# Kernel tuning notes

Hardware: AMD Instinct MI355X
Metric: run time of the kernel (lower is better)

The kernel has to match this reference:

```python
import jax, jax.numpy as jnp
import numpy as np

N = 100000   # nodes
E = 1600000  # edges (avg degree 16)
D = 128      # input_dim == output_dim (residual requires equality)
BN_EPS = 1e-5


def setup_inputs() -> dict:
    key = jax.random.key(0)
    ks = jax.random.split(key, 8)
    X = jax.random.normal(ks[0], (N, D), dtype=jnp.float32)
    E_X = jax.random.normal(ks[1], (E, D), dtype=jnp.float32)
    snorm_n = jax.random.uniform(ks[2], (N, 1), dtype=jnp.float32)
    snorm_e = jax.random.uniform(ks[3], (E, 1), dtype=jnp.float32)
    src = jax.random.randint(ks[4], (E,), 0, N, dtype=jnp.int32)
    dst = jax.random.randint(ks[5], (E,), 0, N, dtype=jnp.int32)
    # Linear A and B parameters (torch nn.Linear: y = x @ W.T + b)
    scale = 1.0 / np.sqrt(D)
    A_w = jax.random.uniform(ks[6], (D, D), dtype=jnp.float32, minval=-scale, maxval=scale)
    B_w = jax.random.uniform(ks[7], (D, D), dtype=jnp.float32, minval=-scale, maxval=scale)
    A_b = jnp.zeros((D,), jnp.float32)
    B_b = jnp.zeros((D,), jnp.float32)
    # BatchNorm1d affine params (training mode -> batch stats)
    gamma = jnp.ones((D,), jnp.float32)
    beta = jnp.zeros((D,), jnp.float32)
    return {"X": X, "E_X": E_X, "snorm_n": snorm_n, "snorm_e": snorm_e,
            "src": src, "dst": dst, "A_w": A_w, "A_b": A_b,
            "B_w": B_w, "B_b": B_b, "gamma": gamma, "beta": beta}


def reference(X, E_X, snorm_n, snorm_e, src, dst, A_w, A_b, B_w, B_b, gamma, beta):
    AX = X @ A_w.T + A_b                       # [N, D]
    BX = X @ B_w.T + B_b                       # [N, D]
    # message: gather BX at edge sources; reduce: sum into destinations
    msgs = BX[src]                             # [E, D] irregular gather
    agg = jax.ops.segment_sum(msgs, dst, num_segments=N)  # [N, D]
    # DGL custom reduce only fires for nodes with in-degree > 0;
    # zero-in-degree nodes keep H = X
    indeg = jax.ops.segment_sum(jnp.ones((E,), X.dtype), dst, num_segments=N)
    H = jnp.where(indeg[:, None] > 0, AX + agg, X)
    H = H * snorm_n
    # BatchNorm1d (training mode: biased batch statistics)
    mean = jnp.mean(H, axis=0)
    var = jnp.mean((H - mean) ** 2, axis=0)
    H = (H - mean) * jax.lax.rsqrt(var + BN_EPS) * gamma + beta
    H = jax.nn.relu(H)
    H = X + H                                  # residual
    return (H, E_X)
```

## Files before the change

### kernel.cpp

```cpp
#include <hip/hip_runtime.h>

#define D 128
#define NNODES 100000
#define NEDGES 1600000
#define BN_EPS 1e-5f
#define NB_STATS 2048
#define NBLK_P 391
#define NTILES 1563

#define OFF_AX16   0
#define OFF_BX16   6400000
#define OFF_H16    12800000
#define OFF_ESRC   19200000
#define OFF_ORDER  20800000
#define OFF_INDEG  22400000
#define OFF_LEXC   22510000
#define OFF_BPART  22620000
#define OFF_BSCAN  22621000
#define OFF_PSUM   22622000
#define OFF_PSQ    22900000
#define OFF_SCALE  23200000
#define OFF_SHIFT  23200128
#define WS_NEED_BYTES 92900000ull

#define MAIN_GEMM 512
#define MAIN_EDGE 2048
#define MAIN_AGG  2048
#define MAIN_FIN  2048

typedef __attribute__((ext_vector_type(8))) short bf16x8;
typedef __attribute__((ext_vector_type(4))) float f32x4;

static __device__ __forceinline__ unsigned short f2bf(float f) {
    unsigned int u = __float_as_uint(f);
    u = (u + 0x7FFF + ((u >> 16) & 1)) >> 16;
    return (unsigned short)u;
}
static __device__ __forceinline__ float bf_lo(unsigned v) {
    return __uint_as_float(v << 16);
}
static __device__ __forceinline__ float bf_hi(unsigned v) {
    return __uint_as_float(v & 0xFFFF0000u);
}
static __device__ __forceinline__ bf16x8 pack8(float4 a, float4 b) {
    union { uint4 u; bf16x8 v; } r;
    r.u.x = (unsigned)f2bf(a.x) | ((unsigned)f2bf(a.y) << 16);
    r.u.y = (unsigned)f2bf(a.z) | ((unsigned)f2bf(a.w) << 16);
    r.u.z = (unsigned)f2bf(b.x) | ((unsigned)f2bf(b.y) << 16);
    r.u.w = (unsigned)f2bf(b.z) | ((unsigned)f2bf(b.w) << 16);
    return r.v;
}
static __device__ __forceinline__ uint2 packu2(float a0, float a1,
                                               float a2, float a3) {
    uint2 r;
    r.x = (unsigned)f2bf(a0) | ((unsigned)f2bf(a1) << 16);
    r.y = (unsigned)f2bf(a2) | ((unsigned)f2bf(a3) << 16);
    return r;
}

__global__ __launch_bounds__(256, 2) void gemm2_kernel(
    const float* __restrict__ X,
    const float* __restrict__ Aw, const float* __restrict__ Ab,
    const float* __restrict__ Bw, const float* __restrict__ Bb,
    unsigned short* __restrict__ AX16, unsigned short* __restrict__ BX16)
{
    __shared__ unsigned short Xs[64][136];

    const int w    = threadIdx.x >> 6;
    const int lane = threadIdx.x & 63;
    const bool isB = (w >> 1);
    const int colbase = (w & 1) * 64;
    const int bn   = lane & 15;
    const int kg   = lane >> 4;

    const float* __restrict__ Wm   = isB ? Bw : Aw;
    const float* __restrict__ bias = isB ? Bb : Ab;
    unsigned short* __restrict__ Y = isB ? BX16 : AX16;

    bf16x8 wf[4][4];
#pragma unroll
    for (int ks = 0; ks < 4; ++ks)
#pragma unroll
        for (int ct = 0; ct < 4; ++ct) {
            const int d = colbase + ct * 16 + bn;
            const int k = ks * 32 + kg * 8;
            const float4* wp = (const float4*)&Wm[d * D + k];
            wf[ks][ct] = pack8(wp[0], wp[1]);
        }

    float bias4[4];
#pragma unroll
    for (int ct = 0; ct < 4; ++ct) bias4[ct] = bias[colbase + ct * 16 + bn];

    for (int t = blockIdx.x; t < NTILES; t += MAIN_GEMM) {
        const int row0 = t * 64;
        for (int c = threadIdx.x; c < 1024; c += 256) {
            const int r   = c >> 4;
            const int col = (c & 15) * 8;
            const int row = min(row0 + r, NNODES - 1);
            const float4* xp = (const float4*)&X[(size_t)row * D + col];
            const float4 x0 = xp[0], x1 = xp[1];
            union { uint4 u; } pk;
            pk.u.x = (unsigned)f2bf(x0.x) | ((unsigned)f2bf(x0.y) << 16);
            pk.u.y = (unsigned)f2bf(x0.z) | ((unsigned)f2bf(x0.w) << 16);
            pk.u.z = (unsigned)f2bf(x1.x) | ((unsigned)f2bf(x1.y) << 16);
            pk.u.w = (unsigned)f2bf(x1.z) | ((unsigned)f2bf(x1.w) << 16);
            *(uint4*)&Xs[r][col] = pk.u;
        }
        __syncthreads();

        f32x4 acc[4][4];
#pragma unroll
        for (int rt = 0; rt < 4; ++rt)
#pragma unroll
            for (int ct = 0; ct < 4; ++ct)
                acc[rt][ct] = (f32x4){0.f, 0.f, 0.f, 0.f};

#pragma unroll
        for (int ks = 0; ks < 4; ++ks) {
            bf16x8 a[4];
#pragma unroll
            for (int rt = 0; rt < 4; ++rt)
                a[rt] = *(const bf16x8*)&Xs[rt * 16 + bn][ks * 32 + kg * 8];
#pragma unroll
            for (int rt = 0; rt < 4; ++rt)
#pragma unroll
                for (int ct = 0; ct < 4; ++ct)
                    acc[rt][ct] = __builtin_amdgcn_mfma_f32_16x16x32_bf16(
                        a[rt], wf[ks][ct], acc[rt][ct], 0, 0, 0);
        }
        __syncthreads();

#pragma unroll
        for (int rt = 0; rt < 4; ++rt) {
#pragma unroll
            for (int r = 0; r < 4; ++r) {
                const int row = row0 + rt * 16 + kg * 4 + r;
                if (row < NNODES) {
                    unsigned short* yrow = Y + (size_t)row * D + colbase;
#pragma unroll
                    for (int ct = 0; ct < 4; ++ct)
                        yrow[ct * 16 + bn] = f2bf(acc[rt][ct][r] + bias4[ct]);
                }
            }
        }
    }
}

__global__ __launch_bounds__(256) void hist_kernel(
    const int* __restrict__ dst, int* __restrict__ indeg,
    int* __restrict__ order)
{
    for (int e = blockIdx.x * 256 + threadIdx.x; e < NEDGES;
         e += MAIN_EDGE * 256)
        order[e] = atomicAdd(&indeg[dst[e]], 1);
}

__global__ __launch_bounds__(256) void scan1_kernel(
    const int* __restrict__ indeg, int* __restrict__ lexc,
    int* __restrict__ bpart)
{
    __shared__ int ls[256];
    const int i = blockIdx.x * 256 + threadIdx.x;
    const int v = (i < NNODES) ? indeg[i] : 0;
    ls[threadIdx.x] = v;
    __syncthreads();
    for (int off = 1; off < 256; off <<= 1) {
        int u = (threadIdx.x >= off) ? ls[threadIdx.x - off] : 0;
        __syncthreads();
        ls[threadIdx.x] += u;
        __syncthreads();
    }
    if (i < NNODES) lexc[i] = ls[threadIdx.x] - v;
    if (threadIdx.x == 255) bpart[blockIdx.x] = ls[255];
}

__global__ __launch_bounds__(512) void scan2_kernel(
    const int* __restrict__ bpart, int* __restrict__ bscan)
{
    __shared__ int ls[512];
    const int t = threadIdx.x;
    const int v = (t < NBLK_P) ? bpart[t] : 0;
    ls[t] = v;
    __syncthreads();
    for (int off = 1; off < 512; off <<= 1) {
        int u = (t >= off) ? ls[t - off] : 0;
        __syncthreads();
        ls[t] += u;
        __syncthreads();
    }
    if (t < NBLK_P) bscan[t] = ls[t] - v;
}

__global__ __launch_bounds__(256) void fill_kernel(
    const int* __restrict__ src, const int* __restrict__ dst,
    const int* __restrict__ bscan, const int* __restrict__ lexc,
    const int* __restrict__ order, int* __restrict__ esrc)
{
    for (int e = blockIdx.x * 256 + threadIdx.x; e < NEDGES;
         e += MAIN_EDGE * 256) {
        const int v = dst[e];
        esrc[bscan[v >> 8] + lexc[v] + order[e]] = src[e];
    }
}

__global__ __launch_bounds__(256, 8) void agg_kernel(
    const uint2* __restrict__ AX2, const uint2* __restrict__ BX2,
    const float4* __restrict__ X4, const float* __restrict__ snorm,
    const int* __restrict__ bscan, const int* __restrict__ lexc,
    const int* __restrict__ indeg, const int* __restrict__ esrc,
    uint2* __restrict__ H2, float* __restrict__ psum,
    float* __restrict__ psq)
{
    const int w    = threadIdx.x >> 6;
    const int lane = threadIdx.x & 63;
    const int half = lane >> 5;
    const int hl   = lane & 31;
    float s0=0.f,s1=0.f,s2=0.f,s3=0.f, q0=0.f,q1=0.f,q2=0.f,q3=0.f;

    const int wid = blockIdx.x * 4 + w;
    for (int base = wid * 2; base < NNODES; base += MAIN_AGG * 8) {
        const int i = base + half;
        if (i < NNODES) {
            float a0, a1, a2, a3;
            const int deg = indeg[i];
            if (deg > 0) {
                const int rs = bscan[i >> 8] + lexc[i];
                const uint2 av = AX2[(size_t)i * 32 + hl];
                a0 = bf_lo(av.x); a1 = bf_hi(av.x);
                a2 = bf_lo(av.y); a3 = bf_hi(av.y);
                int e = rs;
                const int re = rs + deg;
                for (; e + 4 <= re; e += 4) {
                    const uint2 v0 = BX2[(size_t)esrc[e + 0] * 32 + hl];
                    const uint2 v1 = BX2[(size_t)esrc[e + 1] * 32 + hl];
                    const uint2 v2 = BX2[(size_t)esrc[e + 2] * 32 + hl];
                    const uint2 v3 = BX2[(size_t)esrc[e + 3] * 32 + hl];
                    a0 += bf_lo(v0.x)+bf_lo(v1.x)+bf_lo(v2.x)+bf_lo(v3.x);
                    a1 += bf_hi(v0.x)+bf_hi(v1.x)+bf_hi(v2.x)+bf_hi(v3.x);
                    a2 += bf_lo(v0.y)+bf_lo(v1.y)+bf_lo(v2.y)+bf_lo(v3.y);
                    a3 += bf_hi(v0.y)+bf_hi(v1.y)+bf_hi(v2.y)+bf_hi(v3.y);
                }
                for (; e < re; ++e) {
                    const uint2 v = BX2[(size_t)esrc[e] * 32 + hl];
                    a0 += bf_lo(v.x); a1 += bf_hi(v.x);
                    a2 += bf_lo(v.y); a3 += bf_hi(v.y);
                }
            } else {
                float4 x = X4[(size_t)i * 32 + hl];
                a0 = x.x; a1 = x.y; a2 = x.z; a3 = x.w;
            }
            const float sn = snorm[i];
            a0 *= sn; a1 *= sn; a2 *= sn; a3 *= sn;
            H2[(size_t)i * 32 + hl] = packu2(a0, a1, a2, a3);
            s0 += a0; s1 += a1; s2 += a2; s3 += a3;
            q0 += a0*a0; q1 += a1*a1; q2 += a2*a2; q3 += a3*a3;
        }
    }

    __shared__ float sp[4][64][4], sq[4][64][4];
    sp[w][lane][0]=s0; sp[w][lane][1]=s1; sp[w][lane][2]=s2; sp[w][lane][3]=s3;
    sq[w][lane][0]=q0; sq[w][lane][1]=q1; sq[w][lane][2]=q2; sq[w][lane][3]=q3;
    __syncthreads();
    if (threadIdx.x < D) {
        const int c  = threadIdx.x;
        const int l0 = c >> 2;
        const int j  = c & 3;
        float S = 0.f, Q = 0.f;
#pragma unroll
        for (int w2 = 0; w2 < 4; ++w2) {
            S += sp[w2][l0][j] + sp[w2][32 + l0][j];
            Q += sq[w2][l0][j] + sq[w2][32 + l0][j];
        }
        psum[blockIdx.x * D + c] = S;
        psq [blockIdx.x * D + c] = Q;
    }
}

__global__ __launch_bounds__(1024) void bnstats_kernel(
    const float* __restrict__ psum, const float* __restrict__ psq,
    const float* __restrict__ gamma, const float* __restrict__ beta,
    float* __restrict__ scale, float* __restrict__ shift)
{
    const int c = threadIdx.x & 127;
    const int g = threadIdx.x >> 7;
    float s = 0.f, q = 0.f;
    for (int b = g; b < NB_STATS; b += 8) {
        s += psum[b * D + c];
        q += psq [b * D + c];
    }
    __shared__ float ls[8][D], lq[8][D];
    ls[g][c] = s;
    lq[g][c] = q;
    __syncthreads();
    if (threadIdx.x < D) {
        float S = 0.f, Q = 0.f;
#pragma unroll
        for (int g2 = 0; g2 < 8; ++g2) { S += ls[g2][c]; Q += lq[g2][c]; }
        const float inv_n = 1.0f / (float)NNODES;
        float mean = S * inv_n;
        float var  = Q * inv_n - mean * mean;
        float sc   = rsqrtf(var + BN_EPS) * gamma[c];
        scale[c] = sc;
        shift[c] = beta[c] - mean * sc;
    }
}

__global__ __launch_bounds__(256) void final_kernel(
    const uint2* __restrict__ H2, const float* __restrict__ X,
    const float* __restrict__ scale, const float* __restrict__ shift,
    float* __restrict__ out)
{
    const int total = NNODES * D / 4;
    for (int i = blockIdx.x * 256 + threadIdx.x; i < total;
         i += MAIN_FIN * 256) {
        const uint2 hv = H2[i];
        float4 x = ((const float4*)X)[i];
        int d0 = (i * 4) & 127;
        float4 r;
        r.x = x.x + fmaxf(0.f, bf_lo(hv.x) * scale[d0 + 0] + shift[d0 + 0]);
        r.y = x.y + fmaxf(0.f, bf_hi(hv.x) * scale[d0 + 1] + shift[d0 + 1]);
        r.z = x.z + fmaxf(0.f, bf_lo(hv.y) * scale[d0 + 2] + shift[d0 + 2]);
        r.w = x.w + fmaxf(0.f, bf_hi(hv.y) * scale[d0 + 3] + shift[d0 + 3]);
        ((float4*)out)[i] = r;
    }
}

__global__ __launch_bounds__(256) void copy_kernel(
    const float4* __restrict__ s, float4* __restrict__ d, long n)
{
    const long stride = (long)gridDim.x * 256;
    for (long i = (long)blockIdx.x * 256 + threadIdx.x; i < n; i += stride)
        d[i] = s[i];
}

extern "C" void kernel_launch(void* const* d_in, const int* in_sizes, int n_in,
                              void* d_out, int out_size, void* d_ws, size_t ws_size,
                              hipStream_t stream)
{
    const float* X       = (const float*)d_in[0];
    const float* E_X     = (const float*)d_in[1];
    const float* snorm_n = (const float*)d_in[2];
    const int*   src     = (const int*)d_in[4];
    const int*   dst     = (const int*)d_in[5];
    const float* A_w     = (const float*)d_in[6];
    const float* A_b     = (const float*)d_in[7];
    const float* B_w     = (const float*)d_in[8];
    const float* B_b     = (const float*)d_in[9];
    const float* gamma   = (const float*)d_in[10];
    const float* beta    = (const float*)d_in[11];

    float* out = (float*)d_out;
    const bool use_ws = (ws_size >= WS_NEED_BYTES);
    float* sb = use_ws ? (float*)d_ws : (out + (size_t)NNODES * D);

    unsigned short* AX16  = (unsigned short*)(sb + OFF_AX16);
    unsigned short* BX16  = (unsigned short*)(sb + OFF_BX16);
    unsigned short* H16   = (unsigned short*)(sb + OFF_H16);
    int*            esrc  = (int*)(sb + OFF_ESRC);
    int*            order = (int*)(sb + OFF_ORDER);
    int*            indeg = (int*)(sb + OFF_INDEG);
    int*            lexc  = (int*)(sb + OFF_LEXC);
    int*            bpart = (int*)(sb + OFF_BPART);
    int*            bscan = (int*)(sb + OFF_BSCAN);
    float*          psum  = sb + OFF_PSUM;
    float*          psq   = sb + OFF_PSQ;
    float*          scale = sb + OFF_SCALE;
    float*          shift = sb + OFF_SHIFT;

    hipMemsetAsync(indeg, 0, NNODES * sizeof(int), stream);

    gemm2_kernel<<<MAIN_GEMM, 256, 0, stream>>>(
        X, A_w, A_b, B_w, B_b, AX16, BX16);
    hist_kernel<<<MAIN_EDGE, 256, 0, stream>>>(dst, indeg, order);
    scan1_kernel<<<NBLK_P, 256, 0, stream>>>(indeg, lexc, bpart);
    scan2_kernel<<<1, 512, 0, stream>>>(bpart, bscan);
    fill_kernel<<<MAIN_EDGE, 256, 0, stream>>>(
        src, dst, bscan, lexc, order, esrc);
    agg_kernel<<<MAIN_AGG, 256, 0, stream>>>(
        (const uint2*)AX16, (const uint2*)BX16, (const float4*)X, snorm_n,
        bscan, lexc, indeg, esrc, (uint2*)H16, psum, psq);
    bnstats_kernel<<<1, 1024, 0, stream>>>(psum, psq, gamma, beta,
                                           scale, shift);
    final_kernel<<<MAIN_FIN, 256, 0, stream>>>(
        (const uint2*)H16, X, scale, shift, out);

    copy_kernel<<<4096, 256, 0, stream>>>(
        (const float4*)E_X, (float4*)(out + (size_t)NNODES * D),
        (long)NEDGES * D / 4);
}
```

Baseline: 667.0 us.

## Fuse in-degree histogram into GEMM kernel via extra warp, use memcpy for E_X

```diff
diff --git a/kernel.cpp b/kernel.cpp
--- a/kernel.cpp
+++ b/kernel.cpp
@@ -7,6 +7,7 @@
 #define NB_STATS 2048
 #define NBLK_P 391
 #define NTILES 1563
+#define EPB    3125
 
 #define OFF_AX16   0
 #define OFF_BX16   6400000
@@ -58,102 +59,121 @@
     return r;
 }
 
-__global__ __launch_bounds__(256, 2) void gemm2_kernel(
+__global__ __launch_bounds__(320, 2) void gemm2_kernel(
     const float* __restrict__ X,
     const float* __restrict__ Aw, const float* __restrict__ Ab,
     const float* __restrict__ Bw, const float* __restrict__ Bb,
-    unsigned short* __restrict__ AX16, unsigned short* __restrict__ BX16)
+    unsigned short* __restrict__ AX16, unsigned short* __restrict__ BX16,
+    const int* __restrict__ dst, int* __restrict__ indeg,
+    int* __restrict__ order)
 {
     __shared__ unsigned short Xs[64][136];
 
     const int w    = threadIdx.x >> 6;
     const int lane = threadIdx.x & 63;
-    const bool isB = (w >> 1);
+    const bool isB = (w >> 1) & 1;
     const int colbase = (w & 1) * 64;
     const int bn   = lane & 15;
     const int kg   = lane >> 4;
 
-    const float* __restrict__ Wm   = isB ? Bw : Aw;
-    const float* __restrict__ bias = isB ? Bb : Ab;
+    int       enext = blockIdx.x * EPB;
+    const int eend  = enext + EPB;
+
+    bf16x8 wf[4][4];
+    float bias4[4];
     unsigned short* __restrict__ Y = isB ? BX16 : AX16;
-
-    bf16x8 wf[4][4];
-#pragma unroll
-    for (int ks = 0; ks < 4; ++ks)
-#pragma unroll
-        for (int ct = 0; ct < 4; ++ct) {
-            const int d = colbase + ct * 16 + bn;
-            const int k = ks * 32 + kg * 8;
-            const float4* wp = (const float4*)&Wm[d * D + k];
-            wf[ks][ct] = pack8(wp[0], wp[1]);
-        }
-
-    float bias4[4];
-#pragma unroll
-    for (int ct = 0; ct < 4; ++ct) bias4[ct] = bias[colbase + ct * 16 + bn];
+    if (w < 4) {
+        const float* __restrict__ Wm   = isB ? Bw : Aw;
+        const float* __restrict__ bias = isB ? Bb : Ab;
+#pragma unroll
+        for (int ks = 0; ks < 4; ++ks)
+#pragma unroll
+            for (int ct = 0; ct < 4; ++ct) {
+                const int d = colbase + ct * 16 + bn;
+                const int k = ks * 32 + kg * 8;
+                const float4* wp = (const float4*)&Wm[d * D + k];
+                wf[ks][ct] = pack8(wp[0], wp[1]);
+            }
+#pragma unroll
+        for (int ct = 0; ct < 4; ++ct)
+            bias4[ct] = bias[colbase + ct * 16 + bn];
+    }
 
     for (int t = blockIdx.x; t < NTILES; t += MAIN_GEMM) {
         const int row0 = t * 64;
-        for (int c = threadIdx.x; c < 1024; c += 256) {
-            const int r   = c >> 4;
-            const int col = (c & 15) * 8;
-            const int row = min(row0 + r, NNODES - 1);
-            const float4* xp = (const float4*)&X[(size_t)row * D + col];
-            const float4 x0 = xp[0], x1 = xp[1];
-            union { uint4 u; } pk;
-            pk.u.x = (unsigned)f2bf(x0.x) | ((unsigned)f2bf(x0.y) << 16);
-            pk.u.y = (unsigned)f2bf(x0.z) | ((unsigned)f2bf(x0.w) << 16);
-            pk.u.z = (unsigned)f2bf(x1.x) | ((unsigned)f2bf(x1.y) << 16);
-            pk.u.w = (unsigned)f2bf(x1.z) | ((unsigned)f2bf(x1.w) << 16);
-            *(uint4*)&Xs[r][col] = pk.u;
+        if (w < 4) {
+            for (int c = threadIdx.x; c < 1024; c += 256) {
+                const int r   = c >> 4;
+                const int col = (c & 15) * 8;
+                const int row = min(row0 + r, NNODES - 1);
+                const float4* xp = (const float4*)&X[(size_t)row * D + col];
+                const float4 x0 = xp[0], x1 = xp[1];
+                uint4 pk;
+                pk.x = (unsigned)f2bf(x0.x) | ((unsigned)f2bf(x0.y) << 16);
+                pk.y = (unsigned)f2bf(x0.z) | ((unsigned)f2bf(x0.w) << 16);
+                pk.z = (unsigned)f2bf(x1.x) | ((unsigned)f2bf(x1.y) << 16);
+                pk.w = (unsigned)f2bf(x1.z) | ((unsigned)f2bf(x1.w) << 16);
+                *(uint4*)&Xs[r][col] = pk;
+            }
         }
         __syncthreads();
 
-        f32x4 acc[4][4];
-#pragma unroll
-        for (int rt = 0; rt < 4; ++rt)
-#pragma unroll
-            for (int ct = 0; ct < 4; ++ct)
-                acc[rt][ct] = (f32x4){0.f, 0.f, 0.f, 0.f};
-
-#pragma unroll
-        for (int ks = 0; ks < 4; ++ks) {
-            bf16x8 a[4];
+        if (w < 4) {
+            f32x4 acc[4][4];
 #pragma unroll
             for (int rt = 0; rt < 4; ++rt)
-                a[rt] = *(const bf16x8*)&Xs[rt * 16 + bn][ks * 32 + kg * 8];
-#pragma unroll
-            for (int rt = 0; rt < 4; ++rt)
 #pragma unroll
                 for (int ct = 0; ct < 4; ++ct)
-                    acc[rt][ct] = __builtin_amdgcn_mfma_f32_16x16x32_bf16(
-                        a[rt], wf[ks][ct], acc[rt][ct], 0, 0, 0);
+                    acc[rt][ct] = (f32x4){0.f, 0.f, 0.f, 0.f};
+
+#pragma unroll
+            for (int ks = 0; ks < 4; ++ks) {
+                bf16x8 a[4];
+#pragma unroll
+                for (int rt = 0; rt < 4; ++rt)
+                    a[rt] = *(const bf16x8*)
+                        &Xs[rt * 16 + bn][ks * 32 + kg * 8];
+#pragma unroll
+                for (int rt = 0; rt < 4; ++rt)
+#pragma unroll
+                    for (int ct = 0; ct < 4; ++ct)
+                        acc[rt][ct] =
+                            __builtin_amdgcn_mfma_f32_16x16x32_bf16(
+                                a[rt], wf[ks][ct], acc[rt][ct], 0, 0, 0);
+            }
+            __syncthreads();
+
+#pragma unroll
+            for (int rt = 0; rt < 4; ++rt) {
+#pragma unroll
+                for (int r = 0; r < 4; ++r) {
+                    const int row = row0 + rt * 16 + kg * 4 + r;
+                    if (row < NNODES) {
+                        unsigned short* yrow =
+                            Y + (size_t)row * D + colbase;
+#pragma unroll
+                        for (int ct = 0; ct < 4; ++ct)
+                            yrow[ct * 16 + bn] =
+                                f2bf(acc[rt][ct][r] + bias4[ct]);
+                    }
+                }
+            }
+        } else {
+            const int lim = min(enext + 1024, eend);
+            for (int idx = enext + lane; idx < lim; idx += 64) {
+                const int dv = dst[idx];
+                order[idx] = atomicAdd(&indeg[dv], 1);
+            }
+            enext = lim;
+            __syncthreads();
         }
-        __syncthreads();
-
-#pragma unroll
-        for (int rt = 0; rt < 4; ++rt) {
-#pragma unroll
-            for (int r = 0; r < 4; ++r) {
-                const int row = row0 + rt * 16 + kg * 4 + r;
-                if (row < NNODES) {
-                    unsigned short* yrow = Y + (size_t)row * D + colbase;
-#pragma unroll
-                    for (int ct = 0; ct < 4; ++ct)
-                        yrow[ct * 16 + bn] = f2bf(acc[rt][ct][r] + bias4[ct]);
-                }
-            }
+    }
+    if (w == 4) {
+        for (int idx = enext + lane; idx < eend; idx += 64) {
+            const int dv = dst[idx];
+            order[idx] = atomicAdd(&indeg[dv], 1);
         }
     }
-}
-
-__global__ __launch_bounds__(256) void hist_kernel(
-    const int* __restrict__ dst, int* __restrict__ indeg,
-    int* __restrict__ order)
-{
-    for (int e = blockIdx.x * 256 + threadIdx.x; e < NEDGES;
-         e += MAIN_EDGE * 256)
-        order[e] = atomicAdd(&indeg[dst[e]], 1);
 }
 
 __global__ __launch_bounds__(256) void scan1_kernel(
@@ -231,11 +251,35 @@
                 a2 = bf_lo(av.y); a3 = bf_hi(av.y);
                 int e = rs;
                 const int re = rs + deg;
+                for (; e + 8 <= re; e += 8) {
+                    const int i0 = esrc[e + 0], i1 = esrc[e + 1];
+                    const int i2 = esrc[e + 2], i3 = esrc[e + 3];
+                    const int i4 = esrc[e + 4], i5 = esrc[e + 5];
+                    const int i6 = esrc[e + 6], i7 = esrc[e + 7];
+                    const uint2 v0 = BX2[(size_t)i0 * 32 + hl];
+                    const uint2 v1 = BX2[(size_t)i1 * 32 + hl];
+                    const uint2 v2 = BX2[(size_t)i2 * 32 + hl];
+                    const uint2 v3 = BX2[(size_t)i3 * 32 + hl];
+                    const uint2 v4 = BX2[(size_t)i4 * 32 + hl];
+                    const uint2 v5 = BX2[(size_t)i5 * 32 + hl];
+                    const uint2 v6 = BX2[(size_t)i6 * 32 + hl];
+                    const uint2 v7 = BX2[(size_t)i7 * 32 + hl];
+                    a0 += bf_lo(v0.x)+bf_lo(v1.x)+bf_lo(v2.x)+bf_lo(v3.x)
+                        + bf_lo(v4.x)+bf_lo(v5.x)+bf_lo(v6.x)+bf_lo(v7.x);
+                    a1 += bf_hi(v0.x)+bf_hi(v1.x)+bf_hi(v2.x)+bf_hi(v3.x)
+                        + bf_hi(v4.x)+bf_hi(v5.x)+bf_hi(v6.x)+bf_hi(v7.x);
+                    a2 += bf_lo(v0.y)+bf_lo(v1.y)+bf_lo(v2.y)+bf_lo(v3.y)
+                        + bf_lo(v4.y)+bf_lo(v5.y)+bf_lo(v6.y)+bf_lo(v7.y);
+                    a3 += bf_hi(v0.y)+bf_hi(v1.y)+bf_hi(v2.y)+bf_hi(v3.y)
+                        + bf_hi(v4.y)+bf_hi(v5.y)+bf_hi(v6.y)+bf_hi(v7.y);
+                }
                 for (; e + 4 <= re; e += 4) {
-                    const uint2 v0 = BX2[(size_t)esrc[e + 0] * 32 + hl];
-                    const uint2 v1 = BX2[(size_t)esrc[e + 1] * 32 + hl];
-                    const uint2 v2 = BX2[(size_t)esrc[e + 2] * 32 + hl];
-                    const uint2 v3 = BX2[(size_t)esrc[e + 3] * 32 + hl];
+                    const int i0 = esrc[e + 0], i1 = esrc[e + 1];
+                    const int i2 = esrc[e + 2], i3 = esrc[e + 3];
+                    const uint2 v0 = BX2[(size_t)i0 * 32 + hl];
+                    const uint2 v1 = BX2[(size_t)i1 * 32 + hl];
+                    const uint2 v2 = BX2[(size_t)i2 * 32 + hl];
+                    const uint2 v3 = BX2[(size_t)i3 * 32 + hl];
                     a0 += bf_lo(v0.x)+bf_lo(v1.x)+bf_lo(v2.x)+bf_lo(v3.x);
                     a1 += bf_hi(v0.x)+bf_hi(v1.x)+bf_hi(v2.x)+bf_hi(v3.x);
                     a2 += bf_lo(v0.y)+bf_lo(v1.y)+bf_lo(v2.y)+bf_lo(v3.y);
@@ -326,14 +370,6 @@
     }
 }
 
-__global__ __launch_bounds__(256) void copy_kernel(
-    const float4* __restrict__ s, float4* __restrict__ d, long n)
-{
-    const long stride = (long)gridDim.x * 256;
-    for (long i = (long)blockIdx.x * 256 + threadIdx.x; i < n; i += stride)
-        d[i] = s[i];
-}
-
 extern "C" void kernel_launch(void* const* d_in, const int* in_sizes, int n_in,
                               void* d_out, int out_size, void* d_ws, size_t ws_size,
                               hipStream_t stream)
@@ -370,9 +406,8 @@
 
     hipMemsetAsync(indeg, 0, NNODES * sizeof(int), stream);
 
-    gemm2_kernel<<<MAIN_GEMM, 256, 0, stream>>>(
-        X, A_w, A_b, B_w, B_b, AX16, BX16);
-    hist_kernel<<<MAIN_EDGE, 256, 0, stream>>>(dst, indeg, order);
+    gemm2_kernel<<<MAIN_GEMM, 320, 0, stream>>>(
+        X, A_w, A_b, B_w, B_b, AX16, BX16, dst, indeg, order);
     scan1_kernel<<<NBLK_P, 256, 0, stream>>>(indeg, lexc, bpart);
     scan2_kernel<<<1, 512, 0, stream>>>(bpart, bscan);
     fill_kernel<<<MAIN_EDGE, 256, 0, stream>>>(
@@ -385,7 +420,7 @@
     final_kernel<<<MAIN_FIN, 256, 0, stream>>>(
         (const uint2*)H16, X, scale, shift, out);
 
-    copy_kernel<<<4096, 256, 0, stream>>>(
-        (const float4*)E_X, (float4*)(out + (size_t)NNODES * D),
-        (long)NEDGES * D / 4);
-}
+    hipMemcpyAsync(out + (size_t)NNODES * D, E_X,
+                   (size_t)NEDGES * D * sizeof(float),
+                   hipMemcpyDeviceToDevice, stream);
+}
```

Result: no change. 679.0 us (+1.8%).
